# Kernel tuning notes

Measured on AMD Instinct MI355X. Metric: run time of the kernel, lower is better.

## Reference

```python
import jax, jax.numpy as jnp
import numpy as np

N_NODES = 50000
N_EDGES = 800000
N_GRAPHS = 128
F_IN = 256
H = 256
DH = 64
NC = 2


def _lin_init(k, fin, fout):
    s = 1.0 / np.sqrt(fin)
    return jax.random.uniform(k, (fin, fout), jnp.float32, -s, s)


def setup_inputs() -> dict:
    key = jax.random.key(0)
    ks = jax.random.split(key, 12)
    x = jax.random.normal(ks[0], (N_NODES, F_IN), jnp.float32)
    edge_index = jax.random.randint(ks[1], (2, N_EDGES), 0, N_NODES, jnp.int32)
    edge_attr = jax.random.uniform(ks[2], (N_EDGES,), jnp.float32)
    batch = jnp.sort(jax.random.randint(ks[3], (N_NODES,), 0, N_GRAPHS, jnp.int32))
    return {
        "x": x, "edge_index": edge_index, "edge_attr": edge_attr, "batch": batch,
        "W1": _lin_init(ks[4], F_IN, H), "b1": jnp.zeros((H,), jnp.float32),
        "W2": _lin_init(ks[5], H, H), "b2": jnp.zeros((H,), jnp.float32),
        "W3": _lin_init(ks[6], H, H), "b3": jnp.zeros((H,), jnp.float32),
        "L1w": _lin_init(ks[7], H, DH), "L1b": jnp.zeros((DH,), jnp.float32),
        "L2w": _lin_init(ks[8], DH, DH // 2), "L2b": jnp.zeros((DH // 2,), jnp.float32),
        "L3w": _lin_init(ks[9], DH // 2, NC), "L3b": jnp.zeros((NC,), jnp.float32),
    }


def reference(x, edge_index, edge_attr, batch, W1, b1, W2, b2, W3, b3,
              L1w, L1b, L2w, L2b, L3w, L3b):
    src, dst = edge_index[0], edge_index[1]
    # GCN normalization with self loops (weight 1): deg includes self-loop
    deg = jax.ops.segment_sum(edge_attr, dst, num_segments=N_NODES) + 1.0
    dinv = jnp.where(deg > 0, jax.lax.rsqrt(deg), 0.0)
    norm = dinv[src] * edge_attr * dinv[dst]          # [E]
    self_coef = dinv * dinv                            # [N], self-loop norm

    def gcn(h, W, b):
        h = h @ W                                      # [N, H]
        agg = jax.ops.segment_sum(norm[:, None] * h[src], dst, num_segments=N_NODES)
        return agg + self_coef[:, None] * h + b

    c1 = gcn(x, W1, b1)
    h = jax.nn.relu(c1)                                # dropout is eval-mode no-op
    c2 = gcn(h, W2, b2)
    h = jax.nn.relu(c2)
    c3 = gcn(h, W3, b3)
    h = jax.nn.relu(c3)

    # global mean pool over graphs
    sums = jax.ops.segment_sum(h, batch, num_segments=N_GRAPHS)
    cnt = jax.ops.segment_sum(jnp.ones((N_NODES,), h.dtype), batch, num_segments=N_GRAPHS)
    pooled = sums / jnp.clip(cnt, 1.0)[:, None]        # [B, H]

    o = jax.nn.relu(pooled @ L1w + L1b)
    o = jax.nn.relu(o @ L2w + L2b)
    out = jax.nn.relu(o @ L3w + L3b)                   # [B, NC]
    return (out, pooled, c1, c2, c3)
```

## Files before the change

### kernel.cpp

```cpp
#include <hip/hip_runtime.h>

#define N_NODES  50000
#define N_EDGES  800000
#define N_GRAPHS 128
#define FDIM     256

typedef __attribute__((ext_vector_type(8))) short short8;
typedef __attribute__((ext_vector_type(4))) float f32x4;

__device__ __forceinline__ unsigned short f2bf(float f) {
    union { float f; unsigned int u; } v; v.f = f;
    unsigned int x = v.u;
    unsigned int r = (x + 0x7FFFu + ((x >> 16) & 1u)) >> 16;
    return (unsigned short)r;
}

__device__ __forceinline__ float bf2f(unsigned short u) {
    union { unsigned int i; float f; } v;
    v.i = ((unsigned int)u) << 16;
    return v.f;
}


__global__ void k_zero(float* deg, int* cnt, int n) {
    int i = blockIdx.x * blockDim.x + threadIdx.x;
    if (i < n) { deg[i] = 0.0f; cnt[i] = 0; }
}

__global__ void k_deg(const int* __restrict__ dst, const float* __restrict__ ea,
                      float* deg, int* cnt, int E) {
    int e = blockIdx.x * blockDim.x + threadIdx.x;
    if (e < E) {
        int d = dst[e];
        atomicAdd(&deg[d], ea[e]);
        atomicAdd(&cnt[d], 1);
    }
}


__global__ __launch_bounds__(1024) void k_scan1(const int* __restrict__ cnt,
                                                const float* __restrict__ deg,
                                                float* __restrict__ dinv,
                                                int* row_ptr, int* partial, int n) {
    __shared__ int buf[2][1024];
    int tid = threadIdx.x;
    int i = blockIdx.x * 1024 + tid;
    if (i < n) dinv[i] = rsqrtf(deg[i] + 1.0f);
    int v = (i < n) ? cnt[i] : 0;
    buf[0][tid] = v;
    __syncthreads();
    int pb = 0;
    for (int off = 1; off < 1024; off <<= 1) {
        int t = buf[pb][tid];
        if (tid >= off) t += buf[pb][tid - off];
        buf[1 - pb][tid] = t;
        pb = 1 - pb;
        __syncthreads();
    }
    int incl = buf[pb][tid];
    if (i < n) row_ptr[i] = incl - v;
    if (tid == 1023) partial[blockIdx.x] = incl;
}

__global__ void k_scan2(int* partial, int nb, int* totalp) {
    int l = threadIdx.x;
    int v = (l < nb) ? partial[l] : 0;
    int orig = v;
    for (int off = 1; off < 64; off <<= 1) {
        int t = __shfl_up(v, off);
        if (l >= off) v += t;
    }
    if (l < nb) partial[l] = v - orig;
    if (l == nb - 1) *totalp = v;
}

__global__ void k_scan3(int* row_ptr, int* cursor, const int* __restrict__ partial, int n) {
    int i = blockIdx.x * blockDim.x + threadIdx.x;
    if (i < n) {
        int v = row_ptr[i] + partial[i >> 10];
        row_ptr[i] = v;
        cursor[i] = v;
    }
}


__global__ void k_scatter(const int* __restrict__ src, const int* __restrict__ dst,
                          const float* __restrict__ ea,
                          const float* __restrict__ dinv,
                          int* cursor, int2* cv, int E) {
    int e = blockIdx.x * blockDim.x + threadIdx.x;
    if (e < E) {
        int d = dst[e];
        int s = src[e];
        int p = atomicAdd(&cursor[d], 1);
        cv[p] = make_int2(s << 9, __float_as_int(ea[e] * dinv[s]));
    }
}

__global__ void k_repack3(const float* __restrict__ W1, const float* __restrict__ W2,
                          const float* __restrict__ W3, unsigned short* __restrict__ Wp) {
    int tid = blockIdx.x * blockDim.x + threadIdx.x;
    int w = tid >> 16;
    int t = tid & 65535;
    const float* W = (w == 0) ? W1 : ((w == 1) ? W2 : W3);
    int j = t & 7;
    int l = (t >> 3) & 63;
    int c = (t >> 9) & 15;
    int s = t >> 13;
    int k = s * 32 + ((l >> 4) * 8) + j;
    int n = c * 16 + (l & 15);
    Wp[tid] = f2bf(W[k * 256 + n]);
}

__global__ void k_xcast(const float* __restrict__ x, unsigned short* __restrict__ Xb, int n4) {
    int i = blockIdx.x * blockDim.x + threadIdx.x;
    if (i < n4) {
        float4 v = ((const float4*)x)[i];
        ((ushort4*)Xb)[i] = make_ushort4(f2bf(v.x), f2bf(v.y), f2bf(v.z), f2bf(v.w));
    }
}

__global__ __launch_bounds__(256) void k_agg_cs(const unsigned short* __restrict__ Hb,
                                                const int* __restrict__ rowptr,
                                                const int2* __restrict__ cv,
                                                const float* __restrict__ dinv,
                                                unsigned short* __restrict__ S,
                                                int M, int rowBlocks) {
    int pass = blockIdx.x / rowBlocks;
    int rb   = blockIdx.x - pass * rowBlocks;
    int wave = threadIdx.x >> 6;
    int lane = threadIdx.x & 63;
    int sub  = lane >> 4;
    int l16  = lane & 15;
    int n = rb * 4 + wave;
    if (n >= M) return;
    unsigned int cb2 = (unsigned int)((pass * 64 + l16 * 4) * 2);
    const char* Hc = (const char*)Hb;

    float a0 = 0.f, a1 = 0.f, a2 = 0.f, a3 = 0.f;
    int e0 = rowptr[n], e1 = rowptr[n + 1];

    int e = e0 + sub;
    for (; e + 12 < e1; e += 16) {
        int2 p0 = cv[e];
        int2 p1 = cv[e + 4];
        int2 p2 = cv[e + 8];
        int2 p3 = cv[e + 12];
        ushort4 h0 = *(const ushort4*)(Hc + ((unsigned int)p0.x + cb2));
        ushort4 h1 = *(const ushort4*)(Hc + ((unsigned int)p1.x + cb2));
        ushort4 h2 = *(const ushort4*)(Hc + ((unsigned int)p2.x + cb2));
        ushort4 h3 = *(const ushort4*)(Hc + ((unsigned int)p3.x + cb2));
        float v0 = __int_as_float(p0.y);
        float v1 = __int_as_float(p1.y);
        float v2 = __int_as_float(p2.y);
        float v3 = __int_as_float(p3.y);
        a0 = fmaf(v0, bf2f(h0.x), a0); a1 = fmaf(v0, bf2f(h0.y), a1);
        a2 = fmaf(v0, bf2f(h0.z), a2); a3 = fmaf(v0, bf2f(h0.w), a3);
        a0 = fmaf(v1, bf2f(h1.x), a0); a1 = fmaf(v1, bf2f(h1.y), a1);
        a2 = fmaf(v1, bf2f(h1.z), a2); a3 = fmaf(v1, bf2f(h1.w), a3);
        a0 = fmaf(v2, bf2f(h2.x), a0); a1 = fmaf(v2, bf2f(h2.y), a1);
        a2 = fmaf(v2, bf2f(h2.z), a2); a3 = fmaf(v2, bf2f(h2.w), a3);
        a0 = fmaf(v3, bf2f(h3.x), a0); a1 = fmaf(v3, bf2f(h3.y), a1);
        a2 = fmaf(v3, bf2f(h3.z), a2); a3 = fmaf(v3, bf2f(h3.w), a3);
    }
    for (; e < e1; e += 4) {
        int2 p = cv[e];
        ushort4 h = *(const ushort4*)(Hc + ((unsigned int)p.x + cb2));
        float v = __int_as_float(p.y);
        a0 = fmaf(v, bf2f(h.x), a0); a1 = fmaf(v, bf2f(h.y), a1);
        a2 = fmaf(v, bf2f(h.z), a2); a3 = fmaf(v, bf2f(h.w), a3);
    }
    a0 += __shfl_xor(a0, 16); a0 += __shfl_xor(a0, 32);
    a1 += __shfl_xor(a1, 16); a1 += __shfl_xor(a1, 32);
    a2 += __shfl_xor(a2, 16); a2 += __shfl_xor(a2, 32);
    a3 += __shfl_xor(a3, 16); a3 += __shfl_xor(a3, 32);

    if (sub == 0) {
        float di = dinv[n];
        float sc = di * di;
        unsigned int rowb = ((unsigned int)n << 9) + cb2;
        ushort4 hn = *(const ushort4*)(Hc + rowb);
        *(ushort4*)((char*)S + rowb) =
            make_ushort4(f2bf(fmaf(di, a0, sc * bf2f(hn.x))),
                         f2bf(fmaf(di, a1, sc * bf2f(hn.y))),
                         f2bf(fmaf(di, a2, sc * bf2f(hn.z))),
                         f2bf(fmaf(di, a3, sc * bf2f(hn.w))));
    }
}

template<bool RELU>
__global__ __launch_bounds__(256) void k_agg(const float* __restrict__ H,
                                             const int* __restrict__ rowptr,
                                             const int2* __restrict__ cv,
                                             const float* __restrict__ dinv,
                                             unsigned short* __restrict__ S, int M) {
    int wave = threadIdx.x >> 6;
    int lane = threadIdx.x & 63;
    int n = blockIdx.x * 4 + wave;
    if (n >= M) return;
    int f4 = lane * 4;

    float a0 = 0.f, a1 = 0.f, a2 = 0.f, a3 = 0.f;
    int e0 = rowptr[n], e1 = rowptr[n + 1];
    for (int e = e0; e < e1; e++) {
        int2 p = cv[e];
        int s = p.x >> 9;
        float v = __int_as_float(p.y);
        float4 h = *(const float4*)(H + (size_t)s * 256 + f4);
        if (RELU) {
            h.x = fmaxf(h.x, 0.f); h.y = fmaxf(h.y, 0.f);
            h.z = fmaxf(h.z, 0.f); h.w = fmaxf(h.w, 0.f);
        }
        a0 = fmaf(v, h.x, a0); a1 = fmaf(v, h.y, a1);
        a2 = fmaf(v, h.z, a2); a3 = fmaf(v, h.w, a3);
    }
    float di = dinv[n];
    float sc = di * di;
    float4 hn = *(const float4*)(H + (size_t)n * 256 + f4);
    if (RELU) {
        hn.x = fmaxf(hn.x, 0.f); hn.y = fmaxf(hn.y, 0.f);
        hn.z = fmaxf(hn.z, 0.f); hn.w = fmaxf(hn.w, 0.f);
    }
    *(ushort4*)(S + (size_t)n * 256 + f4) =
        make_ushort4(f2bf(fmaf(di, a0, sc * hn.x)), f2bf(fmaf(di, a1, sc * hn.y)),
                     f2bf(fmaf(di, a2, sc * hn.z)), f2bf(fmaf(di, a3, sc * hn.w)));
}

template<bool NT>
__global__ __launch_bounds__(256, 2) void k_gemm2(const unsigned short* __restrict__ S,
                                                  const unsigned short* __restrict__ Wp,
                                                  const float* __restrict__ bias,
                                                  float* __restrict__ C,
                                                  unsigned short* __restrict__ Hb,
                                                  int nTiles) {
    int wave = threadIdx.x >> 6;
    int lane = threadIdx.x & 63;
    int q    = lane >> 4;
    int m16  = lane & 15;
    const short8* wp8 = (const short8*)Wp;

    short8 b[8][4];
#pragma unroll
    for (int s = 0; s < 8; s++)
#pragma unroll
        for (int cc = 0; cc < 4; cc++)
            b[s][cc] = wp8[(s * 16 + wave * 4 + cc) * 64 + lane];

    float bv[4];
#pragma unroll
    for (int cc = 0; cc < 4; cc++) bv[cc] = bias[(wave * 4 + cc) * 16 + m16];

#pragma unroll 1
    for (int rt = blockIdx.x; rt < nTiles; rt += gridDim.x) {
        int arow = rt * 16 + m16;
        short8 a[8];
#pragma unroll
        for (int s = 0; s < 8; s++)
            a[s] = *(const short8*)(S + (size_t)arow * 256 + s * 32 + q * 8);

        f32x4 acc[4];
#pragma unroll
        for (int cc = 0; cc < 4; cc++) acc[cc] = (f32x4){0.f, 0.f, 0.f, 0.f};

#pragma unroll
        for (int s = 0; s < 8; s++)
#pragma unroll
            for (int cc = 0; cc < 4; cc++)
                acc[cc] = __builtin_amdgcn_mfma_f32_16x16x32_bf16(a[s], b[s][cc], acc[cc], 0, 0, 0);

        int orow0 = rt * 16 + q * 4;
#pragma unroll
        for (int cc = 0; cc < 4; cc++) {
            int colv = (wave * 4 + cc) * 16 + m16;
#pragma unroll
            for (int r = 0; r < 4; r++) {
                float ov = acc[cc][r] + bv[cc];
                if (NT) __builtin_nontemporal_store(ov, &C[(size_t)(orow0 + r) * 256 + colv]);
                else    C[(size_t)(orow0 + r) * 256 + colv] = ov;
            }
        }
        if (Hb != nullptr) {
#pragma unroll
            for (int cc = 0; cc < 4; cc++) {
                int colv = (wave * 4 + cc) * 16 + m16;
#pragma unroll
                for (int r = 0; r < 4; r++)
                    Hb[(size_t)(orow0 + r) * 256 + colv] = f2bf(fmaxf(acc[cc][r] + bv[cc], 0.f));
            }
        }
    }
}

__global__ __launch_bounds__(1024) void k_pool(const float* __restrict__ C3,
                                               const int* __restrict__ batch, int N,
                                               float* __restrict__ pooled) {
    int g = blockIdx.x;
    __shared__ int range[2];
    __shared__ float part[4][256];
    if (threadIdx.x == 0 && threadIdx.y == 0) {
        int lo = 0, hi = N;
        while (lo < hi) { int mid = (lo + hi) >> 1; if (batch[mid] < g) lo = mid + 1; else hi = mid; }
        range[0] = lo;
        int lo2 = lo, hi2 = N;
        while (lo2 < hi2) { int mid = (lo2 + hi2) >> 1; if (batch[mid] < g + 1) lo2 = mid + 1; else hi2 = mid; }
        range[1] = lo2;
    }
    __syncthreads();
    int start = range[0], end = range[1];
    int f = threadIdx.x;
    float s = 0.f;
    for (int i = start + threadIdx.y; i < end; i += 4)
        s += fmaxf(C3[(size_t)i * 256 + f], 0.f);
    part[threadIdx.y][f] = s;
    __syncthreads();
    if (threadIdx.y == 0) {
        float tot = part[0][f] + part[1][f] + part[2][f] + part[3][f];
        int cnt = end - start;
        pooled[g * 256 + f] = tot / (float)(cnt > 0 ? cnt : 1);
    }
}

__global__ __launch_bounds__(64) void k_mlp(const float* __restrict__ pooled,
                                            const float* __restrict__ L1w,
                                            const float* __restrict__ L1b,
                                            const float* __restrict__ L2w,
                                            const float* __restrict__ L2b,
                                            const float* __restrict__ L3w,
                                            const float* __restrict__ L3b,
                                            float* __restrict__ out) {
    int g = blockIdx.x;
    int j = threadIdx.x;
    __shared__ float o1[64];
    __shared__ float o2[32];
    float s = L1b[j];
    const float* p = pooled + g * 256;
    for (int k = 0; k < 256; k++) s = fmaf(p[k], L1w[k * 64 + j], s);
    o1[j] = fmaxf(s, 0.f);
    __syncthreads();
    if (j < 32) {
        float s2 = L2b[j];
        for (int k = 0; k < 64; k++) s2 = fmaf(o1[k], L2w[k * 32 + j], s2);
        o2[j] = fmaxf(s2, 0.f);
    }
    __syncthreads();
    if (j < 2) {
        float s3 = L3b[j];
        for (int k = 0; k < 32; k++) s3 = fmaf(o2[k], L3w[k * 2 + j], s3);
        out[g * 2 + j] = fmaxf(s3, 0.f);
    }
}

extern "C" void kernel_launch(void* const* d_in, const int* in_sizes, int n_in,
                              void* d_out, int out_size, void* d_ws, size_t ws_size,
                              hipStream_t stream) {
    const float* x   = (const float*)d_in[0];
    const int*   ei  = (const int*)d_in[1];
    const float* ea  = (const float*)d_in[2];
    const int*   bat = (const int*)d_in[3];
    const float* W1  = (const float*)d_in[4];
    const float* b1  = (const float*)d_in[5];
    const float* W2  = (const float*)d_in[6];
    const float* b2  = (const float*)d_in[7];
    const float* W3  = (const float*)d_in[8];
    const float* b3  = (const float*)d_in[9];
    const float* L1w = (const float*)d_in[10];
    const float* L1b = (const float*)d_in[11];
    const float* L2w = (const float*)d_in[12];
    const float* L2b = (const float*)d_in[13];
    const float* L3w = (const float*)d_in[14];
    const float* L3b = (const float*)d_in[15];

    const int N = N_NODES, E = N_EDGES;
    const int* srcp = ei;
    const int* dstp = ei + E;

    float* out_p    = (float*)d_out;
    float* pooled_p = out_p + 256;
    float* c1_p     = out_p + 33024;
    float* c2_p     = c1_p + (size_t)N * FDIM;
    float* c3_p     = c2_p + (size_t)N * FDIM;

    char* ws = (char*)d_ws;
    size_t off = 0;
    unsigned short* Sb  = (unsigned short*)(ws + off); off += (size_t)(N + 64) * FDIM * 2;
    unsigned short* Wp1 = (unsigned short*)(ws + off); off += 65536 * 2;
    unsigned short* Wp2 = (unsigned short*)(ws + off); off += 65536 * 2;
    unsigned short* Wp3 = (unsigned short*)(ws + off); off += 65536 * 2;
    float* dinv    = (float*)(ws + off); off += (size_t)N * 4;
    float* deg     = (float*)(ws + off); off += (size_t)N * 4;
    int*   cnt     = (int*)(ws + off);   off += (size_t)N * 4;
    int*   row_ptr = (int*)(ws + off);   off += ((size_t)N + 16) * 4;
    int*   cursor  = (int*)(ws + off);   off += (size_t)N * 4;
    int2*  cv      = (int2*)(ws + off);  off += (size_t)E * 8;
    int*   partial = (int*)(ws + off);   off += 64 * 4;
    unsigned short* Hb = (unsigned short*)(ws + off); off += (size_t)(N + 64) * FDIM * 2;
    bool use_bf = (ws_size >= off);
    (void)n_in; (void)in_sizes; (void)out_size;

    int nb256 = (N + 255) / 256;
    int eb256 = (E + 255) / 256;
    int nb1024 = (N + 1023) / 1024;

    k_zero<<<nb256, 256, 0, stream>>>(deg, cnt, N);
    k_deg<<<eb256, 256, 0, stream>>>(dstp, ea, deg, cnt, E);
    k_scan1<<<nb1024, 1024, 0, stream>>>(cnt, deg, dinv, row_ptr, partial, N);
    k_scan2<<<1, 64, 0, stream>>>(partial, nb1024, row_ptr + N);
    k_scan3<<<nb256, 256, 0, stream>>>(row_ptr, cursor, partial, N);
    k_scatter<<<eb256, 256, 0, stream>>>(srcp, dstp, ea, dinv, cursor, cv, E);
    k_repack3<<<768, 256, 0, stream>>>(W1, W2, W3, Wp1);

    int rowBlocks   = (N + 3) / 4;
    int agg_grid    = rowBlocks * 4;
    int nTiles      = (N + 15) / 16;
    int gemm_blocks = 512;

    if (use_bf) {
        k_xcast<<<(N * 64 + 255) / 256, 256, 0, stream>>>(x, Hb, N * 64);
        k_agg_cs<<<agg_grid, 256, 0, stream>>>(Hb, row_ptr, cv, dinv, Sb, N, rowBlocks);
        k_gemm2<true><<<gemm_blocks, 256, 0, stream>>>(Sb, Wp1, b1, c1_p, Hb, nTiles);
        k_agg_cs<<<agg_grid, 256, 0, stream>>>(Hb, row_ptr, cv, dinv, Sb, N, rowBlocks);
        k_gemm2<true><<<gemm_blocks, 256, 0, stream>>>(Sb, Wp2, b2, c2_p, Hb, nTiles);
        k_agg_cs<<<agg_grid, 256, 0, stream>>>(Hb, row_ptr, cv, dinv, Sb, N, rowBlocks);
        k_gemm2<false><<<gemm_blocks, 256, 0, stream>>>(Sb, Wp3, b3, c3_p, nullptr, nTiles);
    } else {
        int agg_blocks = (N + 3) / 4;
        k_agg<false><<<agg_blocks, 256, 0, stream>>>(x, row_ptr, cv, dinv, Sb, N);
        k_gemm2<false><<<gemm_blocks, 256, 0, stream>>>(Sb, Wp1, b1, c1_p, nullptr, nTiles);
        k_agg<true><<<agg_blocks, 256, 0, stream>>>(c1_p, row_ptr, cv, dinv, Sb, N);
        k_gemm2<false><<<gemm_blocks, 256, 0, stream>>>(Sb, Wp2, b2, c2_p, nullptr, nTiles);
        k_agg<true><<<agg_blocks, 256, 0, stream>>>(c2_p, row_ptr, cv, dinv, Sb, N);
        k_gemm2<false><<<gemm_blocks, 256, 0, stream>>>(Sb, Wp3, b3, c3_p, nullptr, nTiles);
    }

    dim3 pb(256, 4);
    k_pool<<<N_GRAPHS, pb, 0, stream>>>(c3_p, bat, N, pooled_p);
    k_mlp<<<N_GRAPHS, 64, 0, stream>>>(pooled_p, L1w, L1b, L2w, L2b, L3w, L3b, out_p);
}
```

Measured before the change: 741.3 us.

## Fuse prep kernels, merge scans, fuse pool with MLP, restructure aggregation

Zeroing, x cast to bf16 and weight repacking are merged into one k_prep launch. The two scan fix-up kernels are merged into one, and pooling is fused with the MLP head. Aggregation switches from a four-pass, sub-wave edge split to one full wave per node, where each lane owns four columns and walks all edges serially. The goal is to cut launch overhead and redundant cv reads, at the cost of less edge-level parallelism per node. The non-bf16 fallback path launches k_prep twice and writes the cast into Sb, which looks odd.

```diff
diff --git a/kernel.cpp b/kernel.cpp
--- a/kernel.cpp
+++ b/kernel.cpp
@@ -21,11 +21,38 @@
     return v.f;
 }
 
-
-__global__ void k_zero(float* deg, int* cnt, int n) {
-    int i = blockIdx.x * blockDim.x + threadIdx.x;
-    if (i < n) { deg[i] = 0.0f; cnt[i] = 0; }
-}
+#define ZBLK 196
+#define XBLK 12500
+#define RBLK 768
+
+__global__ __launch_bounds__(256) void k_prep(float* __restrict__ deg, int* __restrict__ cnt,
+                                              const float* __restrict__ x, unsigned short* __restrict__ Xb,
+                                              const float* __restrict__ W1, const float* __restrict__ W2,
+                                              const float* __restrict__ W3, unsigned short* __restrict__ Wp) {
+    int b = blockIdx.x;
+    int tid = threadIdx.x;
+    if (b < ZBLK) {
+        int i = b * 256 + tid;
+        if (i < N_NODES) { deg[i] = 0.0f; cnt[i] = 0; }
+    } else if (b < ZBLK + XBLK) {
+        int i = (b - ZBLK) * 256 + tid;
+        float4 v = ((const float4*)x)[i];
+        ((ushort4*)Xb)[i] = make_ushort4(f2bf(v.x), f2bf(v.y), f2bf(v.z), f2bf(v.w));
+    } else {
+        int t3 = (b - ZBLK - XBLK) * 256 + tid;
+        int w = t3 >> 16;
+        int t = t3 & 65535;
+        const float* W = (w == 0) ? W1 : ((w == 1) ? W2 : W3);
+        int j = t & 7;
+        int l = (t >> 3) & 63;
+        int c = (t >> 9) & 15;
+        int s = t >> 13;
+        int k = s * 32 + ((l >> 4) * 8) + j;
+        int n = c * 16 + (l & 15);
+        Wp[t3] = f2bf(W[k * 256 + n]);
+    }
+}
+
 
 __global__ void k_deg(const int* __restrict__ dst, const float* __restrict__ ea,
                       float* deg, int* cnt, int E) {
@@ -62,25 +89,29 @@
     if (tid == 1023) partial[blockIdx.x] = incl;
 }
 
-__global__ void k_scan2(int* partial, int nb, int* totalp) {
-    int l = threadIdx.x;
-    int v = (l < nb) ? partial[l] : 0;
-    int orig = v;
-    for (int off = 1; off < 64; off <<= 1) {
-        int t = __shfl_up(v, off);
-        if (l >= off) v += t;
-    }
-    if (l < nb) partial[l] = v - orig;
-    if (l == nb - 1) *totalp = v;
-}
-
-__global__ void k_scan3(int* row_ptr, int* cursor, const int* __restrict__ partial, int n) {
-    int i = blockIdx.x * blockDim.x + threadIdx.x;
+__global__ __launch_bounds__(256) void k_scan2(int* row_ptr, int* cursor,
+                                               const int* __restrict__ partial,
+                                               int nb, int n) {
+    __shared__ int pre[64];
+    int tid = threadIdx.x;
+    if (tid < 64) {
+        int v = (tid < nb) ? partial[tid] : 0;
+        for (int off = 1; off < 64; off <<= 1) {
+            int t = __shfl_up(v, off);
+            if (tid >= off) v += t;
+        }
+        pre[tid] = v;
+    }
+    __syncthreads();
+    int i = blockIdx.x * 256 + tid;
     if (i < n) {
-        int v = row_ptr[i] + partial[i >> 10];
+        int b = i >> 10;
+        int add = (b > 0) ? pre[b - 1] : 0;
+        int v = row_ptr[i] + add;
         row_ptr[i] = v;
         cursor[i] = v;
     }
+    if (blockIdx.x == 0 && tid == 0) row_ptr[n] = N_EDGES;
 }
 
 
@@ -97,63 +128,30 @@
     }
 }
 
-__global__ void k_repack3(const float* __restrict__ W1, const float* __restrict__ W2,
-                          const float* __restrict__ W3, unsigned short* __restrict__ Wp) {
-    int tid = blockIdx.x * blockDim.x + threadIdx.x;
-    int w = tid >> 16;
-    int t = tid & 65535;
-    const float* W = (w == 0) ? W1 : ((w == 1) ? W2 : W3);
-    int j = t & 7;
-    int l = (t >> 3) & 63;
-    int c = (t >> 9) & 15;
-    int s = t >> 13;
-    int k = s * 32 + ((l >> 4) * 8) + j;
-    int n = c * 16 + (l & 15);
-    Wp[tid] = f2bf(W[k * 256 + n]);
-}
-
-__global__ void k_xcast(const float* __restrict__ x, unsigned short* __restrict__ Xb, int n4) {
-    int i = blockIdx.x * blockDim.x + threadIdx.x;
-    if (i < n4) {
-        float4 v = ((const float4*)x)[i];
-        ((ushort4*)Xb)[i] = make_ushort4(f2bf(v.x), f2bf(v.y), f2bf(v.z), f2bf(v.w));
-    }
-}
-
-__global__ __launch_bounds__(256) void k_agg_cs(const unsigned short* __restrict__ Hb,
+__global__ __launch_bounds__(256) void k_agg_bf(const unsigned short* __restrict__ Hb,
                                                 const int* __restrict__ rowptr,
                                                 const int2* __restrict__ cv,
                                                 const float* __restrict__ dinv,
-                                                unsigned short* __restrict__ S,
-                                                int M, int rowBlocks) {
-    int pass = blockIdx.x / rowBlocks;
-    int rb   = blockIdx.x - pass * rowBlocks;
+                                                unsigned short* __restrict__ S, int M) {
     int wave = threadIdx.x >> 6;
     int lane = threadIdx.x & 63;
-    int sub  = lane >> 4;
-    int l16  = lane & 15;
-    int n = rb * 4 + wave;
+    int n = blockIdx.x * 4 + wave;
     if (n >= M) return;
-    unsigned int cb2 = (unsigned int)((pass * 64 + l16 * 4) * 2);
+    unsigned int cb2 = (unsigned int)(lane * 8);
     const char* Hc = (const char*)Hb;
 
     float a0 = 0.f, a1 = 0.f, a2 = 0.f, a3 = 0.f;
     int e0 = rowptr[n], e1 = rowptr[n + 1];
-
-    int e = e0 + sub;
-    for (; e + 12 < e1; e += 16) {
-        int2 p0 = cv[e];
-        int2 p1 = cv[e + 4];
-        int2 p2 = cv[e + 8];
-        int2 p3 = cv[e + 12];
+    int e = e0;
+#pragma unroll 1
+    for (; e + 4 <= e1; e += 4) {
+        int2 p0 = cv[e], p1 = cv[e + 1], p2 = cv[e + 2], p3 = cv[e + 3];
         ushort4 h0 = *(const ushort4*)(Hc + ((unsigned int)p0.x + cb2));
         ushort4 h1 = *(const ushort4*)(Hc + ((unsigned int)p1.x + cb2));
         ushort4 h2 = *(const ushort4*)(Hc + ((unsigned int)p2.x + cb2));
         ushort4 h3 = *(const ushort4*)(Hc + ((unsigned int)p3.x + cb2));
-        float v0 = __int_as_float(p0.y);
-        float v1 = __int_as_float(p1.y);
-        float v2 = __int_as_float(p2.y);
-        float v3 = __int_as_float(p3.y);
+        float v0 = __int_as_float(p0.y), v1 = __int_as_float(p1.y);
+        float v2 = __int_as_float(p2.y), v3 = __int_as_float(p3.y);
         a0 = fmaf(v0, bf2f(h0.x), a0); a1 = fmaf(v0, bf2f(h0.y), a1);
         a2 = fmaf(v0, bf2f(h0.z), a2); a3 = fmaf(v0, bf2f(h0.w), a3);
         a0 = fmaf(v1, bf2f(h1.x), a0); a1 = fmaf(v1, bf2f(h1.y), a1);
@@ -163,29 +161,23 @@
         a0 = fmaf(v3, bf2f(h3.x), a0); a1 = fmaf(v3, bf2f(h3.y), a1);
         a2 = fmaf(v3, bf2f(h3.z), a2); a3 = fmaf(v3, bf2f(h3.w), a3);
     }
-    for (; e < e1; e += 4) {
+#pragma unroll 1
+    for (; e < e1; e++) {
         int2 p = cv[e];
         ushort4 h = *(const ushort4*)(Hc + ((unsigned int)p.x + cb2));
         float v = __int_as_float(p.y);
         a0 = fmaf(v, bf2f(h.x), a0); a1 = fmaf(v, bf2f(h.y), a1);
         a2 = fmaf(v, bf2f(h.z), a2); a3 = fmaf(v, bf2f(h.w), a3);
     }
-    a0 += __shfl_xor(a0, 16); a0 += __shfl_xor(a0, 32);
-    a1 += __shfl_xor(a1, 16); a1 += __shfl_xor(a1, 32);
-    a2 += __shfl_xor(a2, 16); a2 += __shfl_xor(a2, 32);
-    a3 += __shfl_xor(a3, 16); a3 += __shfl_xor(a3, 32);
-
-    if (sub == 0) {
-        float di = dinv[n];
-        float sc = di * di;
-        unsigned int rowb = ((unsigned int)n << 9) + cb2;
-        ushort4 hn = *(const ushort4*)(Hc + rowb);
-        *(ushort4*)((char*)S + rowb) =
-            make_ushort4(f2bf(fmaf(di, a0, sc * bf2f(hn.x))),
-                         f2bf(fmaf(di, a1, sc * bf2f(hn.y))),
-                         f2bf(fmaf(di, a2, sc * bf2f(hn.z))),
-                         f2bf(fmaf(di, a3, sc * bf2f(hn.w))));
-    }
+    float di = dinv[n];
+    float sc = di * di;
+    unsigned int rowb = ((unsigned int)n << 9) + cb2;
+    ushort4 hn = *(const ushort4*)(Hc + rowb);
+    *(ushort4*)((char*)S + rowb) =
+        make_ushort4(f2bf(fmaf(di, a0, sc * bf2f(hn.x))),
+                     f2bf(fmaf(di, a1, sc * bf2f(hn.y))),
+                     f2bf(fmaf(di, a2, sc * bf2f(hn.z))),
+                     f2bf(fmaf(di, a3, sc * bf2f(hn.w))));
 }
 
 template<bool RELU>
@@ -291,12 +283,22 @@
     }
 }
 
-__global__ __launch_bounds__(1024) void k_pool(const float* __restrict__ C3,
-                                               const int* __restrict__ batch, int N,
-                                               float* __restrict__ pooled) {
+__global__ __launch_bounds__(1024) void k_poolmlp(const float* __restrict__ C3,
+                                                  const int* __restrict__ batch, int N,
+                                                  float* __restrict__ pooled,
+                                                  const float* __restrict__ L1w,
+                                                  const float* __restrict__ L1b,
+                                                  const float* __restrict__ L2w,
+                                                  const float* __restrict__ L2b,
+                                                  const float* __restrict__ L3w,
+                                                  const float* __restrict__ L3b,
+                                                  float* __restrict__ out) {
     int g = blockIdx.x;
     __shared__ int range[2];
     __shared__ float part[4][256];
+    __shared__ float pl[256];
+    __shared__ float o1[64];
+    __shared__ float o2[32];
     if (threadIdx.x == 0 && threadIdx.y == 0) {
         int lo = 0, hi = N;
         while (lo < hi) { int mid = (lo + hi) >> 1; if (batch[mid] < g) lo = mid + 1; else hi = mid; }
@@ -316,37 +318,27 @@
     if (threadIdx.y == 0) {
         float tot = part[0][f] + part[1][f] + part[2][f] + part[3][f];
         int cnt = end - start;
-        pooled[g * 256 + f] = tot / (float)(cnt > 0 ? cnt : 1);
-    }
-}
-
-__global__ __launch_bounds__(64) void k_mlp(const float* __restrict__ pooled,
-                                            const float* __restrict__ L1w,
-                                            const float* __restrict__ L1b,
-                                            const float* __restrict__ L2w,
-                                            const float* __restrict__ L2b,
-                                            const float* __restrict__ L3w,
-                                            const float* __restrict__ L3b,
-                                            float* __restrict__ out) {
-    int g = blockIdx.x;
-    int j = threadIdx.x;
-    __shared__ float o1[64];
-    __shared__ float o2[32];
-    float s = L1b[j];
-    const float* p = pooled + g * 256;
-    for (int k = 0; k < 256; k++) s = fmaf(p[k], L1w[k * 64 + j], s);
-    o1[j] = fmaxf(s, 0.f);
-    __syncthreads();
-    if (j < 32) {
-        float s2 = L2b[j];
-        for (int k = 0; k < 64; k++) s2 = fmaf(o1[k], L2w[k * 32 + j], s2);
-        o2[j] = fmaxf(s2, 0.f);
-    }
-    __syncthreads();
-    if (j < 2) {
-        float s3 = L3b[j];
-        for (int k = 0; k < 32; k++) s3 = fmaf(o2[k], L3w[k * 2 + j], s3);
-        out[g * 2 + j] = fmaxf(s3, 0.f);
+        float pv = tot / (float)(cnt > 0 ? cnt : 1);
+        pooled[g * 256 + f] = pv;
+        pl[f] = pv;
+    }
+    __syncthreads();
+    if (threadIdx.y == 0 && f < 64) {
+        float s1 = L1b[f];
+        for (int k = 0; k < 256; k++) s1 = fmaf(pl[k], L1w[k * 64 + f], s1);
+        o1[f] = fmaxf(s1, 0.f);
+    }
+    __syncthreads();
+    if (threadIdx.y == 0 && f < 32) {
+        float s2 = L2b[f];
+        for (int k = 0; k < 64; k++) s2 = fmaf(o1[k], L2w[k * 32 + f], s2);
+        o2[f] = fmaxf(s2, 0.f);
+    }
+    __syncthreads();
+    if (threadIdx.y == 0 && f < 2) {
+        float s3 = L3b[f];
+        for (int k = 0; k < 32; k++) s3 = fmaf(o2[k], L3w[k * 2 + f], s3);
+        out[g * 2 + f] = fmaxf(s3, 0.f);
     }
 }
 
@@ -401,29 +393,29 @@
     int eb256 = (E + 255) / 256;
     int nb1024 = (N + 1023) / 1024;
 
-    k_zero<<<nb256, 256, 0, stream>>>(deg, cnt, N);
+    if (use_bf) {
+        k_prep<<<ZBLK + XBLK + RBLK, 256, 0, stream>>>(deg, cnt, x, Hb, W1, W2, W3, Wp1);
+    } else {
+        k_prep<<<ZBLK + RBLK, 256, 0, stream>>>(deg, cnt, x,  (unsigned short*)Sb, W1, W2, W3, Wp1);
+        k_prep<<<ZBLK + XBLK + RBLK, 256, 0, stream>>>(deg, cnt, x, (unsigned short*)Sb, W1, W2, W3, Wp1);
+    }
     k_deg<<<eb256, 256, 0, stream>>>(dstp, ea, deg, cnt, E);
     k_scan1<<<nb1024, 1024, 0, stream>>>(cnt, deg, dinv, row_ptr, partial, N);
-    k_scan2<<<1, 64, 0, stream>>>(partial, nb1024, row_ptr + N);
-    k_scan3<<<nb256, 256, 0, stream>>>(row_ptr, cursor, partial, N);
+    k_scan2<<<nb256, 256, 0, stream>>>(row_ptr, cursor, partial, nb1024, N);
     k_scatter<<<eb256, 256, 0, stream>>>(srcp, dstp, ea, dinv, cursor, cv, E);
-    k_repack3<<<768, 256, 0, stream>>>(W1, W2, W3, Wp1);
-
-    int rowBlocks   = (N + 3) / 4;
-    int agg_grid    = rowBlocks * 4;
-    int nTiles      = (N + 15) / 16;
+
+    int agg_blocks  = (N + 3) / 4;
+    int nTiles      = N / 16;
     int gemm_blocks = 512;
 
     if (use_bf) {
-        k_xcast<<<(N * 64 + 255) / 256, 256, 0, stream>>>(x, Hb, N * 64);
-        k_agg_cs<<<agg_grid, 256, 0, stream>>>(Hb, row_ptr, cv, dinv, Sb, N, rowBlocks);
+        k_agg_bf<<<agg_blocks, 256, 0, stream>>>(Hb, row_ptr, cv, dinv, Sb, N);
         k_gemm2<true><<<gemm_blocks, 256, 0, stream>>>(Sb, Wp1, b1, c1_p, Hb, nTiles);
-        k_agg_cs<<<agg_grid, 256, 0, stream>>>(Hb, row_ptr, cv, dinv, Sb, N, rowBlocks);
+        k_agg_bf<<<agg_blocks, 256, 0, stream>>>(Hb, row_ptr, cv, dinv, Sb, N);
         k_gemm2<true><<<gemm_blocks, 256, 0, stream>>>(Sb, Wp2, b2, c2_p, Hb, nTiles);
-        k_agg_cs<<<agg_grid, 256, 0, stream>>>(Hb, row_ptr, cv, dinv, Sb, N, rowBlocks);
+        k_agg_bf<<<agg_blocks, 256, 0, stream>>>(Hb, row_ptr, cv, dinv, Sb, N);
         k_gemm2<false><<<gemm_blocks, 256, 0, stream>>>(Sb, Wp3, b3, c3_p, nullptr, nTiles);
     } else {
-        int agg_blocks = (N + 3) / 4;
         k_agg<false><<<agg_blocks, 256, 0, stream>>>(x, row_ptr, cv, dinv, Sb, N);
         k_gemm2<false><<<gemm_blocks, 256, 0, stream>>>(Sb, Wp1, b1, c1_p, nullptr, nTiles);
         k_agg<true><<<agg_blocks, 256, 0, stream>>>(c1_p, row_ptr, cv, dinv, Sb, N);
@@ -433,6 +425,6 @@
     }
 
     dim3 pb(256, 4);
-    k_pool<<<N_GRAPHS, pb, 0, stream>>>(c3_p, bat, N, pooled_p);
-    k_mlp<<<N_GRAPHS, 64, 0, stream>>>(pooled_p, L1w, L1b, L2w, L2b, L3w, L3b, out_p);
-}
+    k_poolmlp<<<N_GRAPHS, pb, 0, stream>>>(c3_p, bat, N, pooled_p,
+                                           L1w, L1b, L2w, L2b, L3w, L3b, out_p);
+}
```

New measurement: 606.0 us. 18.3% less time.
